# Kernel optimization log

Hardware: AMD Instinct MI355X
Metric: run time of the kernel (lower is better)

Reference implementation:

```python
import jax, jax.numpy as jnp
import numpy as np

N, E, IN_DIM, OUT_DIM = 50000, 800000, 128, 128
NEG_SLOPE = 0.01  # F.leaky_relu default


def gcn_conv(x, W, b, src, dst, n_nodes):
    """PyG GCNConv: symmetric norm with self-loops, linear (no bias) -> aggregate -> +bias.
    Self-loop contribution added analytically (norm = deg_inv_sqrt[i]^2) instead of
    materializing an extended edge list."""
    h = x @ W.T  # [N, out]
    deg = jnp.zeros((n_nodes,), x.dtype).at[dst].add(1.0) + 1.0  # in-degree incl. self-loop
    dis = jax.lax.rsqrt(deg)  # deg^{-1/2}
    norm = dis[src] * dis[dst]  # [E]
    msgs = h[src] * norm[:, None]  # gather + scale, [E, out]
    agg = jax.ops.segment_sum(msgs, dst, num_segments=n_nodes)  # scatter-add
    agg = agg + h * (dis * dis)[:, None]  # self-loop messages
    return agg + b


def setup_inputs() -> dict:
    key = jax.random.key(0)
    ks = jax.random.split(key, 6)
    x = jax.random.normal(ks[0], (N, IN_DIM), jnp.float32)
    edge_index = jax.random.randint(ks[1], (2, E), 0, N, dtype=jnp.int32)
    batch = jnp.zeros((N,), jnp.int32)
    W1 = jax.random.normal(ks[2], (OUT_DIM, IN_DIM), jnp.float32) * (1.0 / np.sqrt(IN_DIM))
    b1 = jnp.zeros((OUT_DIM,), jnp.float32)
    W2 = jax.random.normal(ks[3], (OUT_DIM, OUT_DIM), jnp.float32) * (1.0 / np.sqrt(OUT_DIM))
    b2 = jnp.zeros((OUT_DIM,), jnp.float32)
    return {"x": x, "edge_index": edge_index, "batch": batch,
            "W1": W1, "b1": b1, "W2": W2, "b2": b2}


def reference(x, edge_index, batch, W1, b1, W2, b2):
    src, dst = edge_index[0], edge_index[1]
    n = x.shape[0]
    h = gcn_conv(x, W1, b1, src, dst, n)
    h = jax.nn.leaky_relu(h, NEG_SLOPE)
    # dropout is identity in eval mode (training=False)
    return gcn_conv(h, W2, b2, src, dst, n)
```

## Files before the change

### kernel.cpp

```cpp
#include <hip/hip_runtime.h>
#include <hip/hip_bf16.h>
#include <hip/hip_fp16.h>

#define DIM 128
#define NCHUNK 256
#define WLD 136

typedef unsigned short u16;
typedef unsigned int u32;
typedef __attribute__((ext_vector_type(8))) short bf16x8;
typedef __attribute__((ext_vector_type(4))) float f32x4;

__device__ __forceinline__ float bfbits2f(u16 u) {
    return __uint_as_float(((u32)u) << 16);
}
__device__ __forceinline__ u16 f2bf(float f) {
    __hip_bfloat16 b = __float2bfloat16(f);
    return *reinterpret_cast<u16*>(&b);
}
__device__ __forceinline__ u32 pack2bf(float lo, float hi) {
    return (u32)f2bf(lo) | ((u32)f2bf(hi) << 16);
}
__device__ __forceinline__ float h16tof(u16 u) {
    __half hh = *reinterpret_cast<__half*>(&u);
    return __half2float(hh);
}
__device__ __forceinline__ u16 ftoh16(float f) {
    __half hh = __float2half(f);
    return *reinterpret_cast<u16*>(&hh);
}

__global__ __launch_bounds__(256) void k_count(const u16* __restrict__ x,
                                               int* __restrict__ flagp,
                                               const int* __restrict__ dst,
                                               int* __restrict__ counts, int E) {
    if (blockIdx.x == 0 && threadIdx.x == 0) {
        int weird = 0;
        for (int i = 0; i < 256; i += 2) {
            u16 v = x[i];
            int e = (v >> 7) & 0xff;
            if ((v & 0x7fff) != 0 && (e >= 133 || e <= 100)) weird++;
        }
        *flagp = (weird > 16) ? 1 : 0;
    }
    int e = blockIdx.x * blockDim.x + threadIdx.x;
    if (e < E) atomicAdd(&counts[dst[e]], 1);
}

__global__ __launch_bounds__(256) void k_chunksum(const int* __restrict__ counts,
                                                  int* __restrict__ chunksum,
                                                  int N, int chunk) {
    __shared__ int r[256];
    int t = threadIdx.x, b = blockIdx.x;
    int idx = b * chunk + t;
    r[t] = (t < chunk && idx < N) ? counts[idx] + 1 : 0;
    __syncthreads();
    for (int off = 128; off > 0; off >>= 1) {
        if (t < off) r[t] += r[t + off];
        __syncthreads();
    }
    if (t == 0) chunksum[b] = r[0];
}

__global__ __launch_bounds__(256) void k_scanbase(const int* __restrict__ chunksum,
                                                  int* __restrict__ chunkbase,
                                                  int* __restrict__ rowptr, int N) {
    __shared__ int sc[256];
    int t = threadIdx.x;
    int v = chunksum[t];
    sc[t] = v;
    __syncthreads();
    for (int off = 1; off < 256; off <<= 1) {
        int add = (t >= off) ? sc[t - off] : 0;
        __syncthreads();
        sc[t] += add;
        __syncthreads();
    }
    chunkbase[t] = sc[t] - v;
    if (t == 255) rowptr[N] = sc[255];
}

__global__ __launch_bounds__(256) void k_rowptr(int* __restrict__ counts,
                                                const int* __restrict__ chunkbase,
                                                int* __restrict__ rowptr,
                                                float* __restrict__ dis,
                                                u32* __restrict__ pay,
                                                int N, int chunk) {
    __shared__ int sc[256];
    int t = threadIdx.x, b = blockIdx.x;
    int idx = b * chunk + t;
    int v = (t < chunk && idx < N) ? counts[idx] + 1 : 0;
    sc[t] = v;
    __syncthreads();
    for (int off = 1; off < 256; off <<= 1) {
        int add = (t >= off) ? sc[t - off] : 0;
        __syncthreads();
        sc[t] += add;
        __syncthreads();
    }
    if (t < chunk && idx < N) {
        rowptr[idx] = chunkbase[b] + sc[t] - v;
        float dv = rsqrtf((float)v);
        dis[idx] = dv;
        pay[idx] = ((u32)idx << 16) | (u32)ftoh16(dv);
        counts[idx] = 0;
    }
}

__global__ __launch_bounds__(256) void k_fill(const int* __restrict__ src,
                                              const int* __restrict__ dst,
                                              const int* __restrict__ rowptr,
                                              int* __restrict__ cursor,
                                              const u32* __restrict__ pay,
                                              u32* __restrict__ elist, int E, int N) {
    int e = blockIdx.x * blockDim.x + threadIdx.x;
    if (e < E) {
        int d = dst[e];
        int r = atomicAdd(&cursor[d], 1);
        elist[rowptr[d] + r] = pay[src[e]];
    } else if (e < E + N) {
        int d = e - E;
        int r = atomicAdd(&cursor[d], 1);
        elist[rowptr[d] + r] = pay[d];
    }
}

__global__ __launch_bounds__(256) void k_gemm(const void* __restrict__ in,
                                              const void* __restrict__ W,
                                              u16* __restrict__ h, int N,
                                              const int* __restrict__ flagp, int in_mode) {
    __shared__ u16 Wsh[128 * WLD];
    const int tid = threadIdx.x;
    const int flag = *flagp;
    const int in_f32 = in_mode ? flag : 0;
    const int n0 = blockIdx.x * 64;

    if (flag) {
        const float* Wf = (const float*)W;
        for (int t = tid; t < 128 * 32; t += 256) {
            int r = t >> 5, c4 = (t & 31) * 4;
            float4 w = *(const float4*)(Wf + r * DIM + c4);
            uint2 pw = make_uint2(pack2bf(w.x, w.y), pack2bf(w.z, w.w));
            *(uint2*)(Wsh + r * WLD + c4) = pw;
        }
    } else {
        const u16* Wu = (const u16*)W;
        for (int t = tid; t < 128 * 16; t += 256) {
            int r = t >> 4, c8 = (t & 15) * 8;
            *(int4*)(Wsh + r * WLD + c8) = *(const int4*)(Wu + r * DIM + c8);
        }
    }

    const int wid = tid >> 6;
    const int lane = tid & 63;
    const int m_base = wid * 16;
    const int idx16 = lane & 15;
    const int koff = (lane >> 4) * 8;
    const int n = n0 + m_base + idx16;

    bf16x8 afrag[4];
    if (in_f32) {
        const float* xf = (const float*)in;
#pragma unroll
        for (int ks = 0; ks < 4; ++ks) {
            if (n < N) {
                const float* p = xf + (size_t)n * DIM + ks * 32 + koff;
                float4 a = *(const float4*)p;
                float4 b = *(const float4*)(p + 4);
                union { bf16x8 v8; u32 w[4]; } cv;
                cv.w[0] = pack2bf(a.x, a.y);
                cv.w[1] = pack2bf(a.z, a.w);
                cv.w[2] = pack2bf(b.x, b.y);
                cv.w[3] = pack2bf(b.z, b.w);
                afrag[ks] = cv.v8;
            } else {
                afrag[ks] = (bf16x8)0;
            }
        }
    } else {
        const u16* xu = (const u16*)in;
#pragma unroll
        for (int ks = 0; ks < 4; ++ks) {
            afrag[ks] = (n < N) ? *(const bf16x8*)(xu + (size_t)n * DIM + ks * 32 + koff)
                                : (bf16x8)0;
        }
    }
    __syncthreads();

    f32x4 acc[8];
#pragma unroll
    for (int ct = 0; ct < 8; ++ct) acc[ct] = (f32x4){0.f, 0.f, 0.f, 0.f};

#pragma unroll
    for (int ct = 0; ct < 8; ++ct) {
#pragma unroll
        for (int ks = 0; ks < 4; ++ks) {
            bf16x8 bfrag = *(const bf16x8*)(Wsh + (ct * 16 + idx16) * WLD + ks * 32 + koff);
            acc[ct] = __builtin_amdgcn_mfma_f32_16x16x32_bf16(afrag[ks], bfrag, acc[ct], 0, 0, 0);
        }
    }

    const int drow = (lane >> 4) * 4;
#pragma unroll
    for (int ct = 0; ct < 8; ++ct) {
#pragma unroll
        for (int r = 0; r < 4; ++r) {
            int row = n0 + m_base + drow + r;
            if (row < N) h[(size_t)row * DIM + ct * 16 + idx16] = f2bf(acc[ct][r]);
        }
    }
}

template <bool RELU, bool OUT_BF16>
__global__ __launch_bounds__(256) void k_agg(const u16* __restrict__ h,
                                             const float* __restrict__ dis,
                                             const int* __restrict__ rowptr,
                                             const u32* __restrict__ elist,
                                             const void* __restrict__ bias,
                                             void* __restrict__ out, int N,
                                             const int* __restrict__ flagp) {
    const int lane = threadIdx.x & 63;
    const int d = blockIdx.x * 4 + (threadIdx.x >> 6);
    if (d >= N) return;
    const int flag = *flagp;
    const int q  = lane >> 4;
    const int cb = (lane & 15) * 8;

    const int start = rowptr[d];
    const int end   = rowptr[d + 1];
    const int last  = end - 1;
    const float dd  = dis[d];

    float acc[8];
#pragma unroll
    for (int k = 0; k < 8; ++k) acc[k] = 0.f;

    for (int j = start; j < end; j += 16) {
        const int i0 = j + q, i1 = i0 + 4, i2 = i0 + 8, i3 = i0 + 12;
        const u32 e0 = elist[i0 <= last ? i0 : last];
        const u32 e1 = elist[i1 <= last ? i1 : last];
        const u32 e2 = elist[i2 <= last ? i2 : last];
        const u32 e3 = elist[i3 <= last ? i3 : last];
        const float w0 = (i0 <= last) ? h16tof((u16)(e0 & 0xffff)) : 0.f;
        const float w1 = (i1 <= last) ? h16tof((u16)(e1 & 0xffff)) : 0.f;
        const float w2 = (i2 <= last) ? h16tof((u16)(e2 & 0xffff)) : 0.f;
        const float w3 = (i3 <= last) ? h16tof((u16)(e3 & 0xffff)) : 0.f;
        const int4 r0 = *(const int4*)(h + ((size_t)(e0 >> 16)) * DIM + cb);
        const int4 r1 = *(const int4*)(h + ((size_t)(e1 >> 16)) * DIM + cb);
        const int4 r2 = *(const int4*)(h + ((size_t)(e2 >> 16)) * DIM + cb);
        const int4 r3 = *(const int4*)(h + ((size_t)(e3 >> 16)) * DIM + cb);
        const u32 v0[4] = {(u32)r0.x, (u32)r0.y, (u32)r0.z, (u32)r0.w};
        const u32 v1[4] = {(u32)r1.x, (u32)r1.y, (u32)r1.z, (u32)r1.w};
        const u32 v2[4] = {(u32)r2.x, (u32)r2.y, (u32)r2.z, (u32)r2.w};
        const u32 v3[4] = {(u32)r3.x, (u32)r3.y, (u32)r3.z, (u32)r3.w};
#pragma unroll
        for (int k = 0; k < 4; ++k) {
            acc[2 * k]     = fmaf(bfbits2f((u16)(v0[k] & 0xffff)), w0, acc[2 * k]);
            acc[2 * k + 1] = fmaf(bfbits2f((u16)(v0[k] >> 16)),    w0, acc[2 * k + 1]);
        }
#pragma unroll
        for (int k = 0; k < 4; ++k) {
            acc[2 * k]     = fmaf(bfbits2f((u16)(v1[k] & 0xffff)), w1, acc[2 * k]);
            acc[2 * k + 1] = fmaf(bfbits2f((u16)(v1[k] >> 16)),    w1, acc[2 * k + 1]);
        }
#pragma unroll
        for (int k = 0; k < 4; ++k) {
            acc[2 * k]     = fmaf(bfbits2f((u16)(v2[k] & 0xffff)), w2, acc[2 * k]);
            acc[2 * k + 1] = fmaf(bfbits2f((u16)(v2[k] >> 16)),    w2, acc[2 * k + 1]);
        }
#pragma unroll
        for (int k = 0; k < 4; ++k) {
            acc[2 * k]     = fmaf(bfbits2f((u16)(v3[k] & 0xffff)), w3, acc[2 * k]);
            acc[2 * k + 1] = fmaf(bfbits2f((u16)(v3[k] >> 16)),    w3, acc[2 * k + 1]);
        }
    }

#pragma unroll
    for (int k = 0; k < 8; ++k) {
        acc[k] += __shfl_xor(acc[k], 16, 64);
        acc[k] += __shfl_xor(acc[k], 32, 64);
    }

    if (q != 0) return;

    float res[8];
#pragma unroll
    for (int k = 0; k < 8; ++k) res[k] = acc[k] * dd;
    if (flag) {
        const float* bf = (const float*)bias;
#pragma unroll
        for (int k = 0; k < 8; ++k) res[k] += bf[cb + k];
    } else {
        const u16* bu = (const u16*)bias;
#pragma unroll
        for (int k = 0; k < 8; ++k) res[k] += bfbits2f(bu[cb + k]);
    }
    if (RELU) {
#pragma unroll
        for (int k = 0; k < 8; ++k) res[k] = res[k] > 0.f ? res[k] : 0.01f * res[k];
    }
    if (OUT_BF16) {
        u32 pk[4];
#pragma unroll
        for (int k = 0; k < 4; ++k) pk[k] = pack2bf(res[2 * k], res[2 * k + 1]);
        *(int4*)((u16*)out + (size_t)d * DIM + cb) = make_int4(pk[0], pk[1], pk[2], pk[3]);
    } else {
        float* op = (float*)out + (size_t)d * DIM + cb;
        *(float4*)op       = make_float4(res[0], res[1], res[2], res[3]);
        *(float4*)(op + 4) = make_float4(res[4], res[5], res[6], res[7]);
    }
}

extern "C" void kernel_launch(void* const* d_in, const int* in_sizes, int n_in,
                              void* d_out, int out_size, void* d_ws, size_t ws_size,
                              hipStream_t stream) {
    const void* x  = d_in[0];
    const int*  ei = (const int*)d_in[1];
    const void* W1 = d_in[3];
    const void* b1 = d_in[4];
    const void* W2 = d_in[5];
    const void* b2 = d_in[6];

    const int N = in_sizes[0] / DIM;
    const int E = in_sizes[1] / 2;
    const int* src = ei;
    const int* dst = ei + E;
    const int chunk = (N + NCHUNK - 1) / NCHUNK;

    char* ws = (char*)d_ws;
    size_t o = 0;
    int*   flagp    = (int*)(ws + o);   o += 256;
    float* dis      = (float*)(ws + o); o += (((size_t)N * 4 + 255) & ~(size_t)255);
    int*   counts   = (int*)(ws + o);   o += (((size_t)N * 4 + 255) & ~(size_t)255);
    int*   rowptr   = (int*)(ws + o);   o += (((size_t)(N + 1) * 4 + 255) & ~(size_t)255);
    u32*   pay      = (u32*)(ws + o);   o += (((size_t)N * 4 + 255) & ~(size_t)255);
    int*   chunksum = (int*)(ws + o);   o += 1024;
    int*   chunkbase= (int*)(ws + o);   o += 1024;
    u32*   elist    = (u32*)(ws + o);   o += (((size_t)(E + N) * 4 + 255) & ~(size_t)255);
    u16*   h        = (u16*)(ws + o);

    const int eblk = (E + 255) / 256;
    const int fblk = (E + N + 255) / 256;
    const int gblk = (N + 63) / 64;
    const int ablk = (N + 3) / 4;

    hipMemsetAsync(counts, 0, (size_t)N * 4, stream);
    k_count<<<eblk, 256, 0, stream>>>((const u16*)x, flagp, dst, counts, E);
    k_chunksum<<<NCHUNK, 256, 0, stream>>>(counts, chunksum, N, chunk);
    k_scanbase<<<1, 256, 0, stream>>>(chunksum, chunkbase, rowptr, N);
    k_rowptr<<<NCHUNK, 256, 0, stream>>>(counts, chunkbase, rowptr, dis, pay, N, chunk);
    k_fill<<<fblk, 256, 0, stream>>>(src, dst, rowptr, counts, pay, elist, E, N);

    u16* act = (u16*)d_out;

    k_gemm<<<gblk, 256, 0, stream>>>(x, W1, h, N, flagp, 1);
    k_agg<true, true><<<ablk, 256, 0, stream>>>(h, dis, rowptr, elist, b1, act, N, flagp);

    k_gemm<<<gblk, 256, 0, stream>>>(act, W2, h, N, flagp, 0);
    k_agg<false, false><<<ablk, 256, 0, stream>>>(h, dis, rowptr, elist, b2, d_out, N, flagp);
}
```

Measured before the change: 251.6 us.

## Fuse degree count into first GEMM launch and record per-edge ranks for atomic-free fill

```diff
diff --git a/kernel.cpp b/kernel.cpp
--- a/kernel.cpp
+++ b/kernel.cpp
@@ -30,110 +30,55 @@
     return *reinterpret_cast<u16*>(&hh);
 }
 
-__global__ __launch_bounds__(256) void k_count(const u16* __restrict__ x,
-                                               int* __restrict__ flagp,
-                                               const int* __restrict__ dst,
-                                               int* __restrict__ counts, int E) {
-    if (blockIdx.x == 0 && threadIdx.x == 0) {
-        int weird = 0;
-        for (int i = 0; i < 256; i += 2) {
-            u16 v = x[i];
-            int e = (v >> 7) & 0xff;
-            if ((v & 0x7fff) != 0 && (e >= 133 || e <= 100)) weird++;
-        }
-        *flagp = (weird > 16) ? 1 : 0;
-    }
-    int e = blockIdx.x * blockDim.x + threadIdx.x;
-    if (e < E) atomicAdd(&counts[dst[e]], 1);
-}
-
-__global__ __launch_bounds__(256) void k_chunksum(const int* __restrict__ counts,
-                                                  int* __restrict__ chunksum,
-                                                  int N, int chunk) {
-    __shared__ int r[256];
-    int t = threadIdx.x, b = blockIdx.x;
-    int idx = b * chunk + t;
-    r[t] = (t < chunk && idx < N) ? counts[idx] + 1 : 0;
-    __syncthreads();
-    for (int off = 128; off > 0; off >>= 1) {
-        if (t < off) r[t] += r[t + off];
-        __syncthreads();
-    }
-    if (t == 0) chunksum[b] = r[0];
-}
-
-__global__ __launch_bounds__(256) void k_scanbase(const int* __restrict__ chunksum,
-                                                  int* __restrict__ chunkbase,
-                                                  int* __restrict__ rowptr, int N) {
-    __shared__ int sc[256];
-    int t = threadIdx.x;
-    int v = chunksum[t];
-    sc[t] = v;
-    __syncthreads();
-    for (int off = 1; off < 256; off <<= 1) {
-        int add = (t >= off) ? sc[t - off] : 0;
-        __syncthreads();
-        sc[t] += add;
-        __syncthreads();
-    }
-    chunkbase[t] = sc[t] - v;
-    if (t == 255) rowptr[N] = sc[255];
-}
-
-__global__ __launch_bounds__(256) void k_rowptr(int* __restrict__ counts,
-                                                const int* __restrict__ chunkbase,
-                                                int* __restrict__ rowptr,
-                                                float* __restrict__ dis,
-                                                u32* __restrict__ pay,
-                                                int N, int chunk) {
-    __shared__ int sc[256];
-    int t = threadIdx.x, b = blockIdx.x;
-    int idx = b * chunk + t;
-    int v = (t < chunk && idx < N) ? counts[idx] + 1 : 0;
-    sc[t] = v;
-    __syncthreads();
-    for (int off = 1; off < 256; off <<= 1) {
-        int add = (t >= off) ? sc[t - off] : 0;
-        __syncthreads();
-        sc[t] += add;
-        __syncthreads();
-    }
-    if (t < chunk && idx < N) {
-        rowptr[idx] = chunkbase[b] + sc[t] - v;
-        float dv = rsqrtf((float)v);
-        dis[idx] = dv;
-        pay[idx] = ((u32)idx << 16) | (u32)ftoh16(dv);
-        counts[idx] = 0;
-    }
-}
-
-__global__ __launch_bounds__(256) void k_fill(const int* __restrict__ src,
-                                              const int* __restrict__ dst,
-                                              const int* __restrict__ rowptr,
-                                              int* __restrict__ cursor,
-                                              const u32* __restrict__ pay,
-                                              u32* __restrict__ elist, int E, int N) {
-    int e = blockIdx.x * blockDim.x + threadIdx.x;
-    if (e < E) {
-        int d = dst[e];
-        int r = atomicAdd(&cursor[d], 1);
-        elist[rowptr[d] + r] = pay[src[e]];
-    } else if (e < E + N) {
-        int d = e - E;
-        int r = atomicAdd(&cursor[d], 1);
-        elist[rowptr[d] + r] = pay[d];
-    }
-}
-
-__global__ __launch_bounds__(256) void k_gemm(const void* __restrict__ in,
-                                              const void* __restrict__ W,
-                                              u16* __restrict__ h, int N,
-                                              const int* __restrict__ flagp, int in_mode) {
+__device__ __forceinline__ int probe_flag_serial(const u16* __restrict__ x) {
+    int weird = 0;
+    for (int i = 0; i < 256; i += 2) {
+        u16 v = x[i];
+        int e = (v >> 7) & 0xff;
+        if ((v & 0x7fff) != 0 && (e >= 133 || e <= 100)) weird++;
+    }
+    return (weird > 16) ? 1 : 0;
+}
+
+__global__ __launch_bounds__(256) void k_gemm_count(const void* __restrict__ in,
+                                                    const void* __restrict__ W,
+                                                    u16* __restrict__ h, int N,
+                                                    const int* __restrict__ dst,
+                                                    int* __restrict__ counts,
+                                                    int* __restrict__ rank, int E,
+                                                    int* __restrict__ flagp,
+                                                    int gblk, int cblk) {
+    const int bid = blockIdx.x;
+    const int tid = threadIdx.x;
+
+    if (bid & 1) {
+        const int cid = bid >> 1;
+        if (cid >= cblk) return;
+        if (cid == 0 && tid == 0) *flagp = probe_flag_serial((const u16*)in);
+        const int base = cid * 1024;
+#pragma unroll
+        for (int k = 0; k < 4; ++k) {
+            int e = base + k * 256 + tid;
+            if (e < E) rank[e] = atomicAdd(&counts[dst[e]], 1);
+        }
+        return;
+    }
+
+    const int gid = bid >> 1;
+    if (gid >= gblk) return;
+
     __shared__ u16 Wsh[128 * WLD];
-    const int tid = threadIdx.x;
-    const int flag = *flagp;
-    const int in_f32 = in_mode ? flag : 0;
-    const int n0 = blockIdx.x * 64;
+    __shared__ int flag_sh;
+    if (tid == 0) flag_sh = 0;
+    __syncthreads();
+    if (tid < 128) {
+        u16 v = ((const u16*)in)[tid * 2];
+        int ex = (v >> 7) & 0xff;
+        if ((v & 0x7fff) != 0 && (ex >= 133 || ex <= 100)) atomicAdd(&flag_sh, 1);
+    }
+    __syncthreads();
+    const int flag = (flag_sh > 16) ? 1 : 0;
+    const int n0 = gid * 64;
 
     if (flag) {
         const float* Wf = (const float*)W;
@@ -159,7 +104,7 @@
     const int n = n0 + m_base + idx16;
 
     bf16x8 afrag[4];
-    if (in_f32) {
+    if (flag) {
         const float* xf = (const float*)in;
 #pragma unroll
         for (int ks = 0; ks < 4; ++ks) {
@@ -184,6 +129,141 @@
             afrag[ks] = (n < N) ? *(const bf16x8*)(xu + (size_t)n * DIM + ks * 32 + koff)
                                 : (bf16x8)0;
         }
+    }
+    __syncthreads();
+
+    f32x4 acc[8];
+#pragma unroll
+    for (int ct = 0; ct < 8; ++ct) acc[ct] = (f32x4){0.f, 0.f, 0.f, 0.f};
+
+#pragma unroll
+    for (int ct = 0; ct < 8; ++ct) {
+#pragma unroll
+        for (int ks = 0; ks < 4; ++ks) {
+            bf16x8 bfrag = *(const bf16x8*)(Wsh + (ct * 16 + idx16) * WLD + ks * 32 + koff);
+            acc[ct] = __builtin_amdgcn_mfma_f32_16x16x32_bf16(afrag[ks], bfrag, acc[ct], 0, 0, 0);
+        }
+    }
+
+    const int drow = (lane >> 4) * 4;
+#pragma unroll
+    for (int ct = 0; ct < 8; ++ct) {
+#pragma unroll
+        for (int r = 0; r < 4; ++r) {
+            int row = n0 + m_base + drow + r;
+            if (row < N) h[(size_t)row * DIM + ct * 16 + idx16] = f2bf(acc[ct][r]);
+        }
+    }
+}
+
+__global__ __launch_bounds__(256) void k_chunksum(const int* __restrict__ counts,
+                                                  int* __restrict__ chunksum,
+                                                  int N, int chunk) {
+    __shared__ int r[256];
+    int t = threadIdx.x, b = blockIdx.x;
+    int idx = b * chunk + t;
+    r[t] = (t < chunk && idx < N) ? counts[idx] + 1 : 0;
+    __syncthreads();
+    for (int off = 128; off > 0; off >>= 1) {
+        if (t < off) r[t] += r[t + off];
+        __syncthreads();
+    }
+    if (t == 0) chunksum[b] = r[0];
+}
+
+__global__ __launch_bounds__(256) void k_rowptr(const int* __restrict__ counts,
+                                                const int* __restrict__ chunksum,
+                                                int* __restrict__ rowptr,
+                                                float* __restrict__ dis,
+                                                u32* __restrict__ pay,
+                                                int N, int chunk) {
+    __shared__ int scb[256];
+    __shared__ int sc[256];
+    int t = threadIdx.x, b = blockIdx.x;
+
+    int cs = chunksum[t];
+    scb[t] = cs;
+    __syncthreads();
+    for (int off = 1; off < 256; off <<= 1) {
+        int add = (t >= off) ? scb[t - off] : 0;
+        __syncthreads();
+        scb[t] += add;
+        __syncthreads();
+    }
+    if (b == 0 && t == 0) rowptr[N] = scb[255];
+    const int base = (b == 0) ? 0 : scb[b - 1];
+
+    int idx = b * chunk + t;
+    int v = (t < chunk && idx < N) ? counts[idx] + 1 : 0;
+    sc[t] = v;
+    __syncthreads();
+    for (int off = 1; off < 256; off <<= 1) {
+        int add = (t >= off) ? sc[t - off] : 0;
+        __syncthreads();
+        sc[t] += add;
+        __syncthreads();
+    }
+    if (t < chunk && idx < N) {
+        rowptr[idx] = base + sc[t] - v;
+        float dv = rsqrtf((float)v);
+        dis[idx] = dv;
+        pay[idx] = ((u32)idx << 16) | (u32)ftoh16(dv);
+    }
+}
+
+__global__ __launch_bounds__(256) void k_fill(const int* __restrict__ src,
+                                              const int* __restrict__ dst,
+                                              const int* __restrict__ rowptr,
+                                              const int* __restrict__ rank,
+                                              const u32* __restrict__ pay,
+                                              u32* __restrict__ elist, int E, int N) {
+    int e = blockIdx.x * blockDim.x + threadIdx.x;
+    if (e < E) {
+        elist[rowptr[dst[e]] + rank[e]] = pay[src[e]];
+    } else if (e < E + N) {
+        int d = e - E;
+        elist[rowptr[d + 1] - 1] = pay[d];
+    }
+}
+
+__global__ __launch_bounds__(256) void k_gemm(const void* __restrict__ in,
+                                              const void* __restrict__ W,
+                                              u16* __restrict__ h, int N,
+                                              const int* __restrict__ flagp) {
+    __shared__ u16 Wsh[128 * WLD];
+    const int tid = threadIdx.x;
+    const int flag = *flagp;
+    const int n0 = blockIdx.x * 64;
+
+    if (flag) {
+        const float* Wf = (const float*)W;
+        for (int t = tid; t < 128 * 32; t += 256) {
+            int r = t >> 5, c4 = (t & 31) * 4;
+            float4 w = *(const float4*)(Wf + r * DIM + c4);
+            uint2 pw = make_uint2(pack2bf(w.x, w.y), pack2bf(w.z, w.w));
+            *(uint2*)(Wsh + r * WLD + c4) = pw;
+        }
+    } else {
+        const u16* Wu = (const u16*)W;
+        for (int t = tid; t < 128 * 16; t += 256) {
+            int r = t >> 4, c8 = (t & 15) * 8;
+            *(int4*)(Wsh + r * WLD + c8) = *(const int4*)(Wu + r * DIM + c8);
+        }
+    }
+
+    const int wid = tid >> 6;
+    const int lane = tid & 63;
+    const int m_base = wid * 16;
+    const int idx16 = lane & 15;
+    const int koff = (lane >> 4) * 8;
+    const int n = n0 + m_base + idx16;
+
+    bf16x8 afrag[4];
+    const u16* xu = (const u16*)in;
+#pragma unroll
+    for (int ks = 0; ks < 4; ++ks) {
+        afrag[ks] = (n < N) ? *(const bf16x8*)(xu + (size_t)n * DIM + ks * 32 + koff)
+                            : (bf16x8)0;
     }
     __syncthreads();
 
@@ -335,27 +415,27 @@
     int*   rowptr   = (int*)(ws + o);   o += (((size_t)(N + 1) * 4 + 255) & ~(size_t)255);
     u32*   pay      = (u32*)(ws + o);   o += (((size_t)N * 4 + 255) & ~(size_t)255);
     int*   chunksum = (int*)(ws + o);   o += 1024;
-    int*   chunkbase= (int*)(ws + o);   o += 1024;
+    int*   rank     = (int*)(ws + o);   o += (((size_t)E * 4 + 255) & ~(size_t)255);
     u32*   elist    = (u32*)(ws + o);   o += (((size_t)(E + N) * 4 + 255) & ~(size_t)255);
     u16*   h        = (u16*)(ws + o);
 
-    const int eblk = (E + 255) / 256;
+    const int gblk = (N + 63) / 64;
+    const int cblk = (E + 1023) / 1024;
+    const int fused_nb = 2 * (gblk > cblk ? gblk : cblk);
     const int fblk = (E + N + 255) / 256;
-    const int gblk = (N + 63) / 64;
     const int ablk = (N + 3) / 4;
 
+    u16* act = (u16*)d_out;
+
     hipMemsetAsync(counts, 0, (size_t)N * 4, stream);
-    k_count<<<eblk, 256, 0, stream>>>((const u16*)x, flagp, dst, counts, E);
+    k_gemm_count<<<fused_nb, 256, 0, stream>>>(x, W1, h, N, dst, counts, rank, E,
+                                               flagp, gblk, cblk);
     k_chunksum<<<NCHUNK, 256, 0, stream>>>(counts, chunksum, N, chunk);
-    k_scanbase<<<1, 256, 0, stream>>>(chunksum, chunkbase, rowptr, N);
-    k_rowptr<<<NCHUNK, 256, 0, stream>>>(counts, chunkbase, rowptr, dis, pay, N, chunk);
-    k_fill<<<fblk, 256, 0, stream>>>(src, dst, rowptr, counts, pay, elist, E, N);
-
-    u16* act = (u16*)d_out;
-
-    k_gemm<<<gblk, 256, 0, stream>>>(x, W1, h, N, flagp, 1);
+    k_rowptr<<<NCHUNK, 256, 0, stream>>>(counts, chunksum, rowptr, dis, pay, N, chunk);
+    k_fill<<<fblk, 256, 0, stream>>>(src, dst, rowptr, rank, pay, elist, E, N);
+
     k_agg<true, true><<<ablk, 256, 0, stream>>>(h, dis, rowptr, elist, b1, act, N, flagp);
 
-    k_gemm<<<gblk, 256, 0, stream>>>(act, W2, h, N, flagp, 0);
+    k_gemm<<<gblk, 256, 0, stream>>>(act, W2, h, N, flagp);
     k_agg<false, false><<<ablk, 256, 0, stream>>>(h, dis, rowptr, elist, b2, d_out, N, flagp);
 }
```

After: 218.9 us, median of 2. 1.15x faster.
